# Kernel tuning notes

Hardware: AMD Instinct MI355X
Metric: run time of the kernel (lower is better)

## Reference

```python
import jax, jax.numpy as jnp
import numpy as np

DIM = 1024
N_HEAD = 16
HEAD_DIM = DIM // N_HEAD  # 64
B, S = 2, 2048


def setup_inputs() -> dict:
    key = jax.random.key(0)
    ks = jax.random.split(key, 10)
    scale = 1.0 / np.sqrt(DIM)
    return {
        "q": jax.random.normal(ks[0], (B, S, DIM), jnp.float32),
        "freqs_cis": jax.random.normal(ks[1], (S, HEAD_DIM // 2, 2), jnp.float32),
        "wq_w": jax.random.normal(ks[2], (DIM, DIM), jnp.float32) * scale,
        "wq_b": jax.random.normal(ks[3], (DIM,), jnp.float32) * 0.01,
        "wk_w": jax.random.normal(ks[4], (DIM, DIM), jnp.float32) * scale,
        "wk_b": jax.random.normal(ks[5], (DIM,), jnp.float32) * 0.01,
        "wv_w": jax.random.normal(ks[6], (DIM, DIM), jnp.float32) * scale,
        "wv_b": jax.random.normal(ks[7], (DIM,), jnp.float32) * 0.01,
        "wo_w": jax.random.normal(ks[8], (DIM, DIM), jnp.float32) * scale,
        "wo_b": jax.random.normal(ks[9], (DIM,), jnp.float32) * 0.01,
    }


def apply_rotary_emb(x, freqs_cis):
    # x: [B, S, H, D]; freqs_cis: [S, D//2, 2]
    xr = x.reshape(*x.shape[:-1], -1, 2)          # [B,S,H,D/2,2]
    fc = freqs_cis[None, :, None, :, :]            # [1,S,1,D/2,2]
    real = xr[..., 0] * fc[..., 0] - xr[..., 1] * fc[..., 1]
    imag = xr[..., 1] * fc[..., 0] + xr[..., 0] * fc[..., 1]
    return jnp.stack([real, imag], axis=-1).reshape(x.shape).astype(x.dtype)


def reference(q, freqs_cis, wq_w, wq_b, wk_w, wk_b, wv_w, wv_b, wo_w, wo_b):
    bsz, seqlen, _ = q.shape
    # fused-style QKV projections (torch Linear: x @ W.T + b)
    qh = (q @ wq_w.T + wq_b).reshape(bsz, seqlen, N_HEAD, HEAD_DIM)
    kh = (q @ wk_w.T + wk_b).reshape(bsz, seqlen, N_HEAD, HEAD_DIM)
    vh = (q @ wv_w.T + wv_b).reshape(bsz, seqlen, N_HEAD, HEAD_DIM)
    qh = apply_rotary_emb(qh, freqs_cis[:seqlen])
    kh = apply_rotary_emb(kh, freqs_cis[:seqlen])
    # SDPA: softmax(q k^T / sqrt(d)) v, no mask, no dropout
    scale = 1.0 / jnp.sqrt(jnp.asarray(HEAD_DIM, qh.dtype))
    scores = jnp.einsum("bqhd,bkhd->bhqk", qh, kh) * scale
    attn = jax.nn.softmax(scores, axis=-1)
    y = jnp.einsum("bhqk,bkhd->bqhd", attn, vh).reshape(bsz, seqlen, DIM)
    return y @ wo_w.T + wo_b
```

## Files before the change

### kernel.cpp

```cpp
#include <hip/hip_runtime.h>
#include <cstdint>
#include <type_traits>

#define SEQ 2048
#define NTOK 4096

typedef unsigned short u16;
typedef __attribute__((ext_vector_type(8))) short bf16x8;
typedef __attribute__((ext_vector_type(4))) short bf16x4;
typedef __attribute__((ext_vector_type(4))) float f32x4;

#define C_SC 0.18033688f

__device__ __forceinline__ float bf2f(u16 u) {
  union { float f; uint32_t i; } c; c.i = ((uint32_t)u) << 16; return c.f;
}
__device__ __forceinline__ u16 f2bf(float f) {
  union { float f; uint32_t i; } c; c.f = f;
  uint32_t r = c.i + 0x7FFF + ((c.i >> 16) & 1);
  return (u16)(r >> 16);
}
__device__ __forceinline__ void gload_lds16(const void* g, void* l) {
  __builtin_amdgcn_global_load_lds(
      (const __attribute__((address_space(1))) uint32_t*)g,
      (__attribute__((address_space(3))) uint32_t*)l, 16, 0, 0);
}
__device__ __forceinline__ bf16x4 tr_read_b16(const u16* p) {
  bf16x4 d;
  auto a = (const __attribute__((address_space(3))) u16*)p;
  asm volatile("ds_read_b64_tr_b16 %0, %1" : "=v"(d) : "v"(a));
  return d;
}

__global__ void prep_kernel(const float* __restrict__ x,
                            const float* __restrict__ wq, const float* __restrict__ wk,
                            const float* __restrict__ wv, const float* __restrict__ wo,
                            const float* __restrict__ qb, const float* __restrict__ kb,
                            const float* __restrict__ vb,
                            u16* __restrict__ Xb, u16* __restrict__ Wqkv,
                            u16* __restrict__ Wo, float* __restrict__ biasq) {
  int gid = blockIdx.x;
  if (gid < 8192) {
    const float* s; u16* d; int i;
    if (gid < 4096)      { s = x;  d = Xb;                  i = gid * 256 + threadIdx.x; }
    else if (gid < 5120) { s = wq; d = Wqkv;                i = (gid - 4096) * 256 + threadIdx.x; }
    else if (gid < 6144) { s = wk; d = Wqkv + 1024 * 1024;  i = (gid - 5120) * 256 + threadIdx.x; }
    else if (gid < 7168) { s = wv; d = Wqkv + 2048 * 1024;  i = (gid - 6144) * 256 + threadIdx.x; }
    else                 { s = wo; d = Wo;                  i = (gid - 7168) * 256 + threadIdx.x; }
    float4 v = ((const float4*)s)[i];
    uint2 o;
    o.x = (uint)f2bf(v.x) | ((uint)f2bf(v.y) << 16);
    o.y = (uint)f2bf(v.z) | ((uint)f2bf(v.w) << 16);
    ((uint2*)d)[i] = o;
  } else {
    int i = (gid - 8192) * 256 + threadIdx.x;
    if (i < 1024) biasq[i] = qb[i];
    else if (i < 2048) biasq[i] = kb[i - 1024];
    else if (i < 3072) biasq[i] = vb[i - 2048];
  }
}

template <typename OT, bool ROPE>
__global__ __launch_bounds__(256) void gemm_bt(
    const u16* __restrict__ A, const u16* __restrict__ Bt,
    const float* __restrict__ bias, OT* __restrict__ C,
    int M, int N, int K, const float* __restrict__ freqs)
{
  __shared__ alignas(16) u16 As[128 * 64];
  __shared__ alignas(16) u16 Bs[128 * 64];
  const int t = threadIdx.x, w = t >> 6, l = t & 63;
  const int lo = l & 15, hi = l >> 4;
  const int m0 = blockIdx.x * 128, n0 = blockIdx.y * 128;
  const int wm = w >> 1, wn = w & 1;
  f32x4 acc[4][4] = {};
  const int srow = t >> 3;
  const int scol = ((t & 7) ^ (srow & 7)) << 3;
  const u16* ga = A + (size_t)(m0 + srow) * K + scol;
  const u16* gb = Bt + (size_t)(n0 + srow) * K + scol;
  char* dA = (char*)As + t * 16;
  char* dB = (char*)Bs + t * 16;
  const int sw = (lo & 7) << 4;
  for (int kt = 0; kt < K; kt += 64) {
    __syncthreads();
#pragma unroll
    for (int j = 0; j < 4; ++j) {
      gload_lds16(ga + (size_t)(32 * j) * K + kt, dA + j * 4096);
      gload_lds16(gb + (size_t)(32 * j) * K + kt, dB + j * 4096);
    }
    __syncthreads();
#pragma unroll
    for (int kk = 0; kk < 2; ++kk) {
      bf16x8 af[4], bfr[4];
#pragma unroll
      for (int mi = 0; mi < 4; ++mi)
        af[mi] = *(const bf16x8*)((const char*)As + (wm * 64 + mi * 16 + lo) * 128
                                  + ((kk * 64 + hi * 16) ^ sw));
#pragma unroll
      for (int ni = 0; ni < 4; ++ni)
        bfr[ni] = *(const bf16x8*)((const char*)Bs + (wn * 64 + ni * 16 + lo) * 128
                                   + ((kk * 64 + hi * 16) ^ sw));
#pragma unroll
      for (int mi = 0; mi < 4; ++mi)
#pragma unroll
        for (int ni = 0; ni < 4; ++ni)
          acc[mi][ni] = __builtin_amdgcn_mfma_f32_16x16x32_bf16(af[mi], bfr[ni], acc[mi][ni], 0, 0, 0);
    }
  }
  const bool do_rope = ROPE && (n0 < 2048);
  const float2* fc = (const float2*)freqs;
#pragma unroll
  for (int mi = 0; mi < 4; ++mi)
#pragma unroll
    for (int ni = 0; ni < 4; ++ni) {
      int col = n0 + wn * 64 + ni * 16 + lo;
      float b = bias[col];
      int pr = (col >> 1) & 31;
#pragma unroll
      for (int r = 0; r < 4; ++r) {
        int row = m0 + wm * 64 + mi * 16 + hi * 4 + r;
        float v = acc[mi][ni][r] + b;
        if (do_rope) {
          float pv = __shfl_xor(v, 1, 64);
          float2 f = fc[(row & (SEQ - 1)) * 32 + pr];
          float fs = (col & 1) ? f.y : -f.y;
          v = v * f.x + pv * fs;
        }
        if constexpr (std::is_same<OT, u16>::value)
          C[(size_t)row * N + col] = f2bf(v);
        else
          C[(size_t)row * N + col] = v;
      }
    }
}

__global__ __launch_bounds__(256, 4) void attn_kernel(const u16* __restrict__ QKV, u16* __restrict__ Y) {
  const int qt = blockIdx.x, bh = blockIdx.y;
  const int b = bh >> 4, h = bh & 15;
  const int t = threadIdx.x, w = t >> 6, l = t & 63;
  const int lo = l & 15, hi = l >> 4;
  const int q0 = qt * 64;
  __shared__ alignas(128) u16 Ks[2][64 * 64];
  __shared__ alignas(128) u16 Vs[2][64 * 64];
  __shared__ alignas(128) u16 Pl[4][1024];

  const u16* Qrow = QKV + (size_t)(b * SEQ + q0 + w * 16 + lo) * 3072 + h * 64;
  bf16x8 qf0 = *(const bf16x8*)(Qrow + hi * 8);
  bf16x8 qf1 = *(const bf16x8*)(Qrow + 32 + hi * 8);

  const short one_bf = (short)0x3F80;
  const bf16x8 ones = {one_bf, one_bf, one_bf, one_bf, one_bf, one_bf, one_bf, one_bf};

  f32x4 acc[4] = {};
  f32x4 accl = {};
  float mr[4];
#pragma unroll
  for (int r = 0; r < 4; ++r) mr[r] = -INFINITY;

  const u16* Kg = QKV + (size_t)b * SEQ * 3072 + 1024 + h * 64;
  const u16* Vg = QKV + (size_t)b * SEQ * 3072 + 2048 + h * 64;
  const int kr = t >> 3;
  const int ksc = (((t & 7) ^ (kr & 7)) << 3);
  const u16* pK1 = Kg + (size_t)kr * 3072 + ksc;
  const int vk = ((t >> 5) << 2) | ((t >> 1) & 3);
  const int vd = (((t >> 3) & 3) << 4) | ((t & 1) << 3);
  const u16* pV1 = Vg + (size_t)vk * 3072 + vd;

  const int sw = (lo & 7) << 4;
  u16* plw = &Pl[w][0];
  const int wbase = ((lo >> 2) << 6) + ((lo & 3) << 4) + (hi << 2);
  const u16* pt = plw + lo * 4;
  auto stage = [&](int buf, int it) {
    const size_t koff = (size_t)it * 64 * 3072;
    char* dK = (char*)&Ks[buf][0] + t * 16;
    char* dV = (char*)&Vs[buf][0] + t * 16;
    gload_lds16(pK1 + koff, dK);
    gload_lds16(pK1 + koff + (size_t)32 * 3072, dK + 4096);
    gload_lds16(pV1 + koff, dV);
    gload_lds16(pV1 + koff + (size_t)32 * 3072, dV + 4096);
  };

  stage(0, 0);
  int cur = 0;
  for (int it = 0; it < SEQ / 64; ++it) {
    __syncthreads();
    if (it + 1 < SEQ / 64) stage(cur ^ 1, it + 1);

    const char* ksb = (const char*)&Ks[cur][0];
    f32x4 sr[4];
#pragma unroll
    for (int fk = 0; fk < 4; ++fk) {
      const char* krow = ksb + (fk * 16 + lo) * 128;
      bf16x8 kb0 = *(const bf16x8*)(krow + ((hi << 4) ^ sw));
      bf16x8 kb1 = *(const bf16x8*)(krow + ((64 + (hi << 4)) ^ sw));
      f32x4 s4 = {};
      s4 = __builtin_amdgcn_mfma_f32_16x16x32_bf16(qf0, kb0, s4, 0, 0, 0);
      sr[fk] = __builtin_amdgcn_mfma_f32_16x16x32_bf16(qf1, kb1, s4, 0, 0, 0);
    }

    float tm[4];
#pragma unroll
    for (int r = 0; r < 4; ++r)
      tm[r] = fmaxf(fmaxf(sr[0][r], sr[1][r]), fmaxf(sr[2][r], sr[3][r])) * C_SC;

    bool ok = (tm[0] <= mr[0] + 8.f) & (tm[1] <= mr[1] + 8.f)
            & (tm[2] <= mr[2] + 8.f) & (tm[3] <= mr[3] + 8.f);
    if (!__all(ok ? 1 : 0)) {
#pragma unroll
      for (int m = 1; m <= 8; m <<= 1)
#pragma unroll
        for (int r = 0; r < 4; ++r)
          tm[r] = fmaxf(tm[r], __shfl_xor(tm[r], m, 64));
#pragma unroll
      for (int r = 0; r < 4; ++r) {
        float mn = fmaxf(mr[r], tm[r]);
        float corr = __builtin_exp2f(mr[r] - mn);
        mr[r] = mn;
        acc[0][r] *= corr; acc[1][r] *= corr; acc[2][r] *= corr; acc[3][r] *= corr;
        accl[r] *= corr;
      }
    }

    float nm0 = -mr[0], nm1 = -mr[1], nm2 = -mr[2], nm3 = -mr[3];
#pragma unroll
    for (int fk = 0; fk < 4; ++fk) {
      float p0 = __builtin_exp2f(fmaf(sr[fk][0], C_SC, nm0));
      float p1 = __builtin_exp2f(fmaf(sr[fk][1], C_SC, nm1));
      float p2 = __builtin_exp2f(fmaf(sr[fk][2], C_SC, nm2));
      float p3 = __builtin_exp2f(fmaf(sr[fk][3], C_SC, nm3));
      uint2 pk;
      asm("v_cvt_pk_bf16_f32 %0, %1, %2" : "=v"(pk.x) : "v"(p0), "v"(p1));
      asm("v_cvt_pk_bf16_f32 %0, %1, %2" : "=v"(pk.y) : "v"(p2), "v"(p3));
      *(uint2*)&plw[wbase + fk * 256] = pk;
    }
    asm volatile("" ::: "memory");

    const u16* vbase = &Vs[cur][0] + hi * 512 + lo * 4;
#pragma unroll
    for (int kk = 0; kk < 2; ++kk) {
      bf16x4 a0 = tr_read_b16(pt + (kk * 8 + hi * 2) * 64);
      bf16x4 a1 = tr_read_b16(pt + (kk * 8 + hi * 2) * 64 + 64);
      bf16x4 ta[4], tb[4];
#pragma unroll
      for (int fd = 0; fd < 4; ++fd) {
        const u16* p0 = vbase + kk * 2048 + fd * 64;
        ta[fd] = tr_read_b16(p0);
        tb[fd] = tr_read_b16(p0 + 256);
      }
      asm volatile("s_waitcnt lgkmcnt(0)" ::: "memory");
      __builtin_amdgcn_sched_barrier(0);
      bf16x8 pa = __builtin_shufflevector(a0, a1, 0, 1, 2, 3, 4, 5, 6, 7);
      accl = __builtin_amdgcn_mfma_f32_16x16x32_bf16(pa, ones, accl, 0, 0, 0);
#pragma unroll
      for (int fd = 0; fd < 4; ++fd) {
        bf16x8 vb = __builtin_shufflevector(ta[fd], tb[fd], 0, 1, 2, 3, 4, 5, 6, 7);
        acc[fd] = __builtin_amdgcn_mfma_f32_16x16x32_bf16(pa, vb, acc[fd], 0, 0, 0);
      }
    }
    cur ^= 1;
  }

  float rinv[4];
#pragma unroll
  for (int r = 0; r < 4; ++r) rinv[r] = __builtin_amdgcn_rcpf(accl[r]);
#pragma unroll
  for (int fd = 0; fd < 4; ++fd)
#pragma unroll
    for (int r = 0; r < 4; ++r) {
      int row = q0 + w * 16 + hi * 4 + r;
      int col = h * 64 + fd * 16 + lo;
      Y[(size_t)(b * SEQ + row) * 1024 + col] = f2bf(acc[fd][r] * rinv[r]);
    }
}

extern "C" void kernel_launch(void* const* d_in, const int* in_sizes, int n_in,
                              void* d_out, int out_size, void* d_ws, size_t ws_size,
                              hipStream_t stream) {
  const float* x     = (const float*)d_in[0];
  const float* freqs = (const float*)d_in[1];
  const float* wq_w  = (const float*)d_in[2];
  const float* wq_b  = (const float*)d_in[3];
  const float* wk_w  = (const float*)d_in[4];
  const float* wk_b  = (const float*)d_in[5];
  const float* wv_w  = (const float*)d_in[6];
  const float* wv_b  = (const float*)d_in[7];
  const float* wo_w  = (const float*)d_in[8];
  const float* wo_b  = (const float*)d_in[9];

  char* ws = (char*)d_ws;
  u16*   Xb    = (u16*)(ws);
  u16*   Wqkv  = (u16*)(ws + 8388608);
  u16*   Wo    = (u16*)(ws + 14680064);
  float* biasq = (float*)(ws + 16777216);
  u16*   QKV   = (u16*)(ws + 16789504);
  u16*   Yb    = (u16*)(ws + 41955328);

  prep_kernel<<<8204, 256, 0, stream>>>(x, wq_w, wk_w, wv_w, wo_w, wq_b, wk_b, wv_b,
                                        Xb, Wqkv, Wo, biasq);
  gemm_bt<u16, true><<<dim3(32, 24), 256, 0, stream>>>(Xb, Wqkv, biasq, QKV, NTOK, 3072, 1024, freqs);
  attn_kernel<<<dim3(SEQ / 64, 32), 256, 0, stream>>>(QKV, Yb);
  gemm_bt<float, false><<<dim3(32, 8), 256, 0, stream>>>(Yb, Wo, wo_b, (float*)d_out, NTOK, 1024, 1024, nullptr);
}
```

Measured before the change: 157.8 us.

## Remap workgroups for XCD locality, single-buffer V, split LDS waits, add priorities

Workgroup ids in both the GEMM and the attention kernel are remapped so that consecutive blocks are spread round-robin across the 8 XCDs, aiming at better L2 reuse. The attention loop drops V double buffering: V is loaded at the start of each iteration and awaited with a partial vmcnt plus a barrier before the PV stage. This halves V LDS and may raise occupancy. All LDS transposed reads for both k-halves are issued up front with a partial lgkmcnt wait, s_setprio is raised around the MFMA sections, and the exp2 builtin is switched to the raw amdgcn version. The risk is that V load latency is now exposed within each iteration.

```diff
diff --git a/kernel.cpp b/kernel.cpp
--- a/kernel.cpp
+++ b/kernel.cpp
@@ -12,9 +12,12 @@
 
 #define C_SC 0.18033688f
 
-__device__ __forceinline__ float bf2f(u16 u) {
-  union { float f; uint32_t i; } c; c.i = ((uint32_t)u) << 16; return c.f;
-}
+#if __has_builtin(__builtin_amdgcn_exp2f)
+#define EXP2F __builtin_amdgcn_exp2f
+#else
+#define EXP2F __builtin_exp2f
+#endif
+
 __device__ __forceinline__ u16 f2bf(float f) {
   union { float f; uint32_t i; } c; c.f = f;
   uint32_t r = c.i + 0x7FFF + ((c.i >> 16) & 1);
@@ -70,7 +73,10 @@
   __shared__ alignas(16) u16 Bs[128 * 64];
   const int t = threadIdx.x, w = t >> 6, l = t & 63;
   const int lo = l & 15, hi = l >> 4;
-  const int m0 = blockIdx.x * 128, n0 = blockIdx.y * 128;
+  const int nwg = gridDim.x * gridDim.y;
+  const int f = blockIdx.y * gridDim.x + blockIdx.x;
+  const int f2 = (f & 7) * (nwg >> 3) + (f >> 3);
+  const int m0 = (f2 % gridDim.x) * 128, n0 = (f2 / gridDim.x) * 128;
   const int wm = w >> 1, wn = w & 1;
   f32x4 acc[4][4] = {};
   const int srow = t >> 3;
@@ -121,9 +127,9 @@
         float v = acc[mi][ni][r] + b;
         if (do_rope) {
           float pv = __shfl_xor(v, 1, 64);
-          float2 f = fc[(row & (SEQ - 1)) * 32 + pr];
-          float fs = (col & 1) ? f.y : -f.y;
-          v = v * f.x + pv * fs;
+          float2 fq = fc[(row & (SEQ - 1)) * 32 + pr];
+          float fs = (col & 1) ? fq.y : -fq.y;
+          v = v * fq.x + pv * fs;
         }
         if constexpr (std::is_same<OT, u16>::value)
           C[(size_t)row * N + col] = f2bf(v);
@@ -134,13 +140,16 @@
 }
 
 __global__ __launch_bounds__(256, 4) void attn_kernel(const u16* __restrict__ QKV, u16* __restrict__ Y) {
-  const int qt = blockIdx.x, bh = blockIdx.y;
+  const int fblk = blockIdx.y * 32 + blockIdx.x;
+  const int f2 = (fblk & 7) * 128 + (fblk >> 3);
+  const int qt = f2 & 31, bh = f2 >> 5;
   const int b = bh >> 4, h = bh & 15;
   const int t = threadIdx.x, w = t >> 6, l = t & 63;
   const int lo = l & 15, hi = l >> 4;
   const int q0 = qt * 64;
+  const int NT = SEQ / 64;
   __shared__ alignas(128) u16 Ks[2][64 * 64];
-  __shared__ alignas(128) u16 Vs[2][64 * 64];
+  __shared__ alignas(128) u16 Vs[64 * 64];
   __shared__ alignas(128) u16 Pl[4][1024];
 
   const u16* Qrow = QKV + (size_t)(b * SEQ + q0 + w * 16 + lo) * 3072 + h * 64;
@@ -169,24 +178,30 @@
   u16* plw = &Pl[w][0];
   const int wbase = ((lo >> 2) << 6) + ((lo & 3) << 4) + (hi << 2);
   const u16* pt = plw + lo * 4;
-  auto stage = [&](int buf, int it) {
-    const size_t koff = (size_t)it * 64 * 3072;
+
+  auto stageK = [&](int buf, int it2) {
+    const size_t koff = (size_t)it2 * 64 * 3072;
     char* dK = (char*)&Ks[buf][0] + t * 16;
-    char* dV = (char*)&Vs[buf][0] + t * 16;
     gload_lds16(pK1 + koff, dK);
     gload_lds16(pK1 + koff + (size_t)32 * 3072, dK + 4096);
+  };
+  auto stageV = [&](int it2) {
+    const size_t koff = (size_t)it2 * 64 * 3072;
+    char* dV = (char*)Vs + t * 16;
     gload_lds16(pV1 + koff, dV);
     gload_lds16(pV1 + koff + (size_t)32 * 3072, dV + 4096);
   };
 
-  stage(0, 0);
+  stageK(0, 0);
   int cur = 0;
-  for (int it = 0; it < SEQ / 64; ++it) {
+  for (int it = 0; it < NT; ++it) {
     __syncthreads();
-    if (it + 1 < SEQ / 64) stage(cur ^ 1, it + 1);
+    stageV(it);
+    if (it + 1 < NT) stageK(cur ^ 1, it + 1);
 
     const char* ksb = (const char*)&Ks[cur][0];
     f32x4 sr[4];
+    __builtin_amdgcn_s_setprio(1);
 #pragma unroll
     for (int fk = 0; fk < 4; ++fk) {
       const char* krow = ksb + (fk * 16 + lo) * 128;
@@ -196,6 +211,7 @@
       s4 = __builtin_amdgcn_mfma_f32_16x16x32_bf16(qf0, kb0, s4, 0, 0, 0);
       sr[fk] = __builtin_amdgcn_mfma_f32_16x16x32_bf16(qf1, kb1, s4, 0, 0, 0);
     }
+    __builtin_amdgcn_s_setprio(0);
 
     float tm[4];
 #pragma unroll
@@ -213,7 +229,7 @@
 #pragma unroll
       for (int r = 0; r < 4; ++r) {
         float mn = fmaxf(mr[r], tm[r]);
-        float corr = __builtin_exp2f(mr[r] - mn);
+        float corr = EXP2F(mr[r] - mn);
         mr[r] = mn;
         acc[0][r] *= corr; acc[1][r] *= corr; acc[2][r] *= corr; acc[3][r] *= corr;
         accl[r] *= corr;
@@ -223,10 +239,10 @@
     float nm0 = -mr[0], nm1 = -mr[1], nm2 = -mr[2], nm3 = -mr[3];
 #pragma unroll
     for (int fk = 0; fk < 4; ++fk) {
-      float p0 = __builtin_exp2f(fmaf(sr[fk][0], C_SC, nm0));
-      float p1 = __builtin_exp2f(fmaf(sr[fk][1], C_SC, nm1));
-      float p2 = __builtin_exp2f(fmaf(sr[fk][2], C_SC, nm2));
-      float p3 = __builtin_exp2f(fmaf(sr[fk][3], C_SC, nm3));
+      float p0 = EXP2F(fmaf(sr[fk][0], C_SC, nm0));
+      float p1 = EXP2F(fmaf(sr[fk][1], C_SC, nm1));
+      float p2 = EXP2F(fmaf(sr[fk][2], C_SC, nm2));
+      float p3 = EXP2F(fmaf(sr[fk][3], C_SC, nm3));
       uint2 pk;
       asm("v_cvt_pk_bf16_f32 %0, %1, %2" : "=v"(pk.x) : "v"(p0), "v"(p1));
       asm("v_cvt_pk_bf16_f32 %0, %1, %2" : "=v"(pk.y) : "v"(p2), "v"(p3));
@@ -234,28 +250,49 @@
     }
     asm volatile("" ::: "memory");
 
-    const u16* vbase = &Vs[cur][0] + hi * 512 + lo * 4;
+    if (it + 1 < NT) { asm volatile("s_waitcnt vmcnt(2)" ::: "memory"); }
+    else             { asm volatile("s_waitcnt vmcnt(0)" ::: "memory"); }
+    __builtin_amdgcn_s_barrier();
+
+    const u16* vbase = &Vs[0] + hi * 512 + lo * 4;
+    bf16x4 a0[2], a1[2], ta[2][4], tb[2][4];
 #pragma unroll
     for (int kk = 0; kk < 2; ++kk) {
-      bf16x4 a0 = tr_read_b16(pt + (kk * 8 + hi * 2) * 64);
-      bf16x4 a1 = tr_read_b16(pt + (kk * 8 + hi * 2) * 64 + 64);
-      bf16x4 ta[4], tb[4];
+      a0[kk] = tr_read_b16(pt + (kk * 8 + hi * 2) * 64);
+      a1[kk] = tr_read_b16(pt + (kk * 8 + hi * 2) * 64 + 64);
 #pragma unroll
       for (int fd = 0; fd < 4; ++fd) {
         const u16* p0 = vbase + kk * 2048 + fd * 64;
-        ta[fd] = tr_read_b16(p0);
-        tb[fd] = tr_read_b16(p0 + 256);
-      }
-      asm volatile("s_waitcnt lgkmcnt(0)" ::: "memory");
-      __builtin_amdgcn_sched_barrier(0);
-      bf16x8 pa = __builtin_shufflevector(a0, a1, 0, 1, 2, 3, 4, 5, 6, 7);
+        ta[kk][fd] = tr_read_b16(p0);
+        tb[kk][fd] = tr_read_b16(p0 + 256);
+      }
+    }
+    asm volatile("s_waitcnt lgkmcnt(10)" ::: "memory");
+    __builtin_amdgcn_sched_barrier(0);
+    __builtin_amdgcn_s_setprio(1);
+    {
+      bf16x8 pa = __builtin_shufflevector(a0[0], a1[0], 0, 1, 2, 3, 4, 5, 6, 7);
       accl = __builtin_amdgcn_mfma_f32_16x16x32_bf16(pa, ones, accl, 0, 0, 0);
 #pragma unroll
       for (int fd = 0; fd < 4; ++fd) {
-        bf16x8 vb = __builtin_shufflevector(ta[fd], tb[fd], 0, 1, 2, 3, 4, 5, 6, 7);
+        bf16x8 vb = __builtin_shufflevector(ta[0][fd], tb[0][fd], 0, 1, 2, 3, 4, 5, 6, 7);
         acc[fd] = __builtin_amdgcn_mfma_f32_16x16x32_bf16(pa, vb, acc[fd], 0, 0, 0);
       }
     }
+    __builtin_amdgcn_s_setprio(0);
+    asm volatile("s_waitcnt lgkmcnt(0)" ::: "memory");
+    __builtin_amdgcn_sched_barrier(0);
+    __builtin_amdgcn_s_setprio(1);
+    {
+      bf16x8 pa = __builtin_shufflevector(a0[1], a1[1], 0, 1, 2, 3, 4, 5, 6, 7);
+      accl = __builtin_amdgcn_mfma_f32_16x16x32_bf16(pa, ones, accl, 0, 0, 0);
+#pragma unroll
+      for (int fd = 0; fd < 4; ++fd) {
+        bf16x8 vb = __builtin_shufflevector(ta[1][fd], tb[1][fd], 0, 1, 2, 3, 4, 5, 6, 7);
+        acc[fd] = __builtin_amdgcn_mfma_f32_16x16x32_bf16(pa, vb, acc[fd], 0, 0, 0);
+      }
+    }
+    __builtin_amdgcn_s_setprio(0);
     cur ^= 1;
   }
 
```

Result: faster. 152.8 us (-3.1%).
